# Optimization experiments

Hardware: AMD Instinct MI355X
Metric: run time of the kernel (lower is better)

The kernel has to match this reference:

```python
import jax, jax.numpy as jnp
import numpy as np

N_EMBD = 1024
N_HEAD = 16
B, T = 4, 2048


def setup_inputs() -> dict:
    key = jax.random.key(0)
    ks = jax.random.split(key, 9)
    s = 1.0 / np.sqrt(N_EMBD)
    d = dict(
        x=jax.random.normal(ks[0], (B, T, N_EMBD), dtype=jnp.float32),
        Wq=jax.random.normal(ks[1], (N_EMBD, N_EMBD), dtype=jnp.float32) * s,
        bq=jax.random.normal(ks[2], (N_EMBD,), dtype=jnp.float32) * 0.01,
        Wk=jax.random.normal(ks[3], (N_EMBD, N_EMBD), dtype=jnp.float32) * s,
        bk=jax.random.normal(ks[4], (N_EMBD,), dtype=jnp.float32) * 0.01,
        Wv=jax.random.normal(ks[5], (N_EMBD, N_EMBD), dtype=jnp.float32) * s,
        bv=jax.random.normal(ks[6], (N_EMBD,), dtype=jnp.float32) * 0.01,
        Wp=jax.random.normal(ks[7], (N_EMBD, N_EMBD), dtype=jnp.float32) * s,
        bp=jax.random.normal(ks[8], (N_EMBD,), dtype=jnp.float32) * 0.01,
    )
    return d


def reference(x, Wq, bq, Wk, bk, Wv, bv, Wp, bp):
    b, t, c = x.shape
    h = N_HEAD
    hd = c // h
    # QKV projections -> [B, H, T, hd]
    def heads(w, bias):
        return (x @ w.T + bias).reshape(b, t, h, hd).transpose(0, 2, 1, 3)
    q = heads(Wq, bq)
    k = heads(Wk, bk)
    v = heads(Wv, bv)
    scale = 1.0 / np.sqrt(hd)
    att = jnp.einsum('bhqd,bhkd->bhqk', q, k) * scale  # [B,H,T,T]
    att = jax.nn.softmax(att, axis=-1)
    y = jnp.einsum('bhqk,bhkd->bhqd', att, v)          # [B,H,T,hd]
    y = y.transpose(0, 2, 1, 3).reshape(b, t, c)
    att_mean = att.mean(axis=1)                        # [B,T,T]
    y = y @ Wp.T + bp
    return y, att_mean
```

## Files before the change

kernel.cpp:

```cpp
#include <hip/hip_runtime.h>
#include <hip/hip_bf16.h>
#include <stdint.h>

#define T_SEQ 2048
#define C_EMB 1024
#define NH    16
#define HD    64
#define BB    4

typedef __attribute__((ext_vector_type(8))) short short8;
typedef __attribute__((ext_vector_type(4))) short short4v;
typedef __attribute__((ext_vector_type(4))) float f32x4;

__device__ __forceinline__ f32x4 mfma16(short8 a, short8 b, f32x4 c) {
  return __builtin_amdgcn_mfma_f32_16x16x32_bf16(a, b, c, 0, 0, 0);
}

__device__ __forceinline__ void load_lds16(const void* g, void* l) {
  __builtin_amdgcn_global_load_lds(
      (__attribute__((address_space(1))) void*)(g),
      (__attribute__((address_space(3))) void*)(l), 16, 0, 0);
}

__device__ __forceinline__ unsigned short f2bf(float f) {
  union { float f; unsigned u; } x; x.f = f;
  unsigned r = x.u + 0x7fffu + ((x.u >> 16) & 1u);
  return (unsigned short)(r >> 16);
}

__device__ __forceinline__ short8 swz_read(const unsigned short* base, int r, int cb) {
  return *(const short8*)((const char*)base + r * 128 + (cb ^ ((r & 7) << 4)));
}

__global__ void cvt4(const float* __restrict__ src, unsigned short* __restrict__ dst, int n) {
  int i = (blockIdx.x * 256 + threadIdx.x) * 4;
  if (i < n) {
    float4 v = *reinterpret_cast<const float4*>(src + i);
    short4v o;
    o[0] = (short)f2bf(v.x); o[1] = (short)f2bf(v.y);
    o[2] = (short)f2bf(v.z); o[3] = (short)f2bf(v.w);
    *reinterpret_cast<short4v*>(dst + i) = o;
  }
}

__global__ void pack_bias(const float* __restrict__ bq, const float* __restrict__ bk,
                          const float* __restrict__ bv, float* __restrict__ out) {
  int i = blockIdx.x * 256 + threadIdx.x;
  float v = (i < 1024) ? bq[i] : (i < 2048 ? bk[i - 1024] : bv[i - 2048]);
  out[i] = v;
}

template <bool OUT_BF16>
__global__ void gemm_bt(const unsigned short* __restrict__ A,
                        const unsigned short* __restrict__ Bw,
                        const float* __restrict__ bias,
                        unsigned short* __restrict__ Cb, float* __restrict__ Cf,
                        int M, int N, int K) {
  __shared__ unsigned short lA[128 * 64];
  __shared__ unsigned short lB[128 * 64];
  const int tid = threadIdx.x;
  const int lane = tid & 63;
  const int w = tid >> 6;
  const int m0 = blockIdx.x * 128;
  const int n0 = blockIdx.y * 128;
  const int wm = (w >> 1) * 64, wn = (w & 1) * 64;

  f32x4 acc[4][4] = {};

  for (int k0 = 0; k0 < K; k0 += 64) {
#pragma unroll
    for (int i = 0; i < 4; ++i) {
      int o = (i * 256 + tid) * 16;
      int row = o >> 7, colb = o & 127;
      load_lds16(A + (size_t)(m0 + row) * K + k0 + (colb >> 1), (char*)lA + o);
      load_lds16(Bw + (size_t)(n0 + row) * K + k0 + (colb >> 1), (char*)lB + o);
    }
    __syncthreads();
#pragma unroll
    for (int kk = 0; kk < 2; ++kk) {
      short8 af[4], bf[4];
#pragma unroll
      for (int mi = 0; mi < 4; ++mi)
        af[mi] = *(const short8*)&lA[(wm + mi * 16 + (lane & 15)) * 64 + kk * 32 + (lane >> 4) * 8];
#pragma unroll
      for (int ni = 0; ni < 4; ++ni)
        bf[ni] = *(const short8*)&lB[(wn + ni * 16 + (lane & 15)) * 64 + kk * 32 + (lane >> 4) * 8];
#pragma unroll
      for (int mi = 0; mi < 4; ++mi)
#pragma unroll
        for (int ni = 0; ni < 4; ++ni)
          acc[mi][ni] = mfma16(af[mi], bf[ni], acc[mi][ni]);
    }
    __syncthreads();
  }
#pragma unroll
  for (int mi = 0; mi < 4; ++mi) {
#pragma unroll
    for (int ni = 0; ni < 4; ++ni) {
#pragma unroll
      for (int r = 0; r < 4; ++r) {
        int m = m0 + wm + mi * 16 + (lane >> 4) * 4 + r;
        int n = n0 + wn + ni * 16 + (lane & 15);
        float v = acc[mi][ni][r] + bias[n];
        if (OUT_BF16) Cb[(size_t)m * N + n] = f2bf(v);
        else          Cf[(size_t)m * N + n] = v;
      }
    }
  }
}

__global__ void vtrans(const unsigned short* __restrict__ qkv, unsigned short* __restrict__ vt) {
  const int tt = blockIdx.x, h = blockIdx.y, b = blockIdx.z;
  const int tid = threadIdx.x;
  __shared__ unsigned short ltile[64][65];
#pragma unroll
  for (int i = 0; i < 2; ++i) {
    int e = i * 2048 + tid * 8;
    int t = e >> 6, d = e & 63;
    short8 v = *(const short8*)(qkv + ((size_t)(b * T_SEQ + tt * 64 + t)) * 3072 + 2048 + h * 64 + d);
#pragma unroll
    for (int j = 0; j < 8; ++j) ltile[d + j][t] = (unsigned short)v[j];
  }
  __syncthreads();
#pragma unroll
  for (int i = 0; i < 2; ++i) {
    int e = i * 2048 + tid * 8;
    int d = e >> 6, t = e & 63;
    short8 sv;
#pragma unroll
    for (int j = 0; j < 8; ++j) sv[j] = (short)ltile[d][t + j];
    *(short8*)(vt + ((size_t)((b * NH + h) * HD + d)) * T_SEQ + tt * 64 + t) = sv;
  }
}

__global__ void flash_fwd(const unsigned short* __restrict__ qkv,
                          const unsigned short* __restrict__ vt,
                          unsigned short* __restrict__ yb,
                          float* __restrict__ mstat, float* __restrict__ lstat) {
  const int qt = blockIdx.x, h = blockIdx.y, b = blockIdx.z;
  const int tid = threadIdx.x, lane = tid & 63, w = tid >> 6;
  __shared__ unsigned short kl[2][64 * 64];
  __shared__ unsigned short vl[2][64 * 64];
  __shared__ unsigned short pl[4][16 * 64];
  const int qbase = qt * 64;
  const float scale = 0.125f;

  short8 qf[2];
  {
    int qr = qbase + w * 16 + (lane & 15);
    const unsigned short* qp = qkv + ((size_t)(b * T_SEQ + qr)) * 3072 + h * 64 + (lane >> 4) * 8;
    qf[0] = *(const short8*)(qp);
    qf[1] = *(const short8*)(qp + 32);
  }

  f32x4 yacc[4] = {};
  float mrow[4], lrow[4];
#pragma unroll
  for (int r = 0; r < 4; ++r) { mrow[r] = -1e30f; lrow[r] = 0.f; }

  auto stage = [&](int buf, int kb) {
#pragma unroll
    for (int i = 0; i < 2; ++i) {
      int o = (i * 256 + tid) * 16;
      int row = o >> 7;
      int colb = (o & 127) ^ ((row & 7) << 4);
      load_lds16(qkv + ((size_t)(b * T_SEQ + kb + row)) * 3072 + 1024 + h * 64 + (colb >> 1),
                 (char*)kl[buf] + o);
      load_lds16(vt + ((size_t)((b * NH + h) * HD + row)) * T_SEQ + kb + (colb >> 1),
                 (char*)vl[buf] + o);
    }
  };

  stage(0, 0);
  __syncthreads();
  int cur = 0;

  for (int kt = 0; kt < T_SEQ / 64; ++kt) {
    if (kt + 1 < T_SEQ / 64) stage(cur ^ 1, (kt + 1) * 64);

    f32x4 s[4] = {};
#pragma unroll
    for (int kk = 0; kk < 2; ++kk) {
#pragma unroll
      for (int ct = 0; ct < 4; ++ct) {
        short8 bfr = swz_read(kl[cur], ct * 16 + (lane & 15), kk * 64 + (lane >> 4) * 16);
        s[ct] = mfma16(qf[kk], bfr, s[ct]);
      }
    }

    float alpha[4];
#pragma unroll
    for (int r = 0; r < 4; ++r) {
      float mx = fmaxf(fmaxf(s[0][r], s[1][r]), fmaxf(s[2][r], s[3][r]));
#pragma unroll
      for (int d = 1; d < 16; d <<= 1) mx = fmaxf(mx, __shfl_xor(mx, d));
      float mt = mx * scale;
      float mnew = fmaxf(mrow[r], mt);
      alpha[r] = __expf(mrow[r] - mnew);
      mrow[r] = mnew;
      float sum = 0.f;
      int pr = (lane >> 4) * 4 + r;
#pragma unroll
      for (int ct = 0; ct < 4; ++ct) {
        float p = __expf(s[ct][r] * scale - mnew);
        sum += p;
        *(unsigned short*)((char*)pl[w] + pr * 128 +
                           ((ct * 32 + (lane & 15) * 2) ^ ((pr & 7) << 4))) = f2bf(p);
      }
#pragma unroll
      for (int d = 1; d < 16; d <<= 1) sum += __shfl_xor(sum, d);
      lrow[r] = lrow[r] * alpha[r] + sum;
    }
#pragma unroll
    for (int dt = 0; dt < 4; ++dt)
#pragma unroll
      for (int r = 0; r < 4; ++r) yacc[dt][r] *= alpha[r];

#pragma unroll
    for (int kk = 0; kk < 2; ++kk) {
      short8 pa = swz_read(pl[w], lane & 15, kk * 64 + (lane >> 4) * 16);
#pragma unroll
      for (int dt = 0; dt < 4; ++dt) {
        short8 bv = swz_read(vl[cur], dt * 16 + (lane & 15), kk * 64 + (lane >> 4) * 16);
        yacc[dt] = mfma16(pa, bv, yacc[dt]);
      }
    }

    __syncthreads();
    cur ^= 1;
  }

#pragma unroll
  for (int r = 0; r < 4; ++r) {
    int qr = qbase + w * 16 + (lane >> 4) * 4 + r;
    float inv = 1.f / lrow[r];
#pragma unroll
    for (int dt = 0; dt < 4; ++dt) {
      float v = yacc[dt][r] * inv;
      yb[((size_t)(b * T_SEQ + qr)) * C_EMB + h * HD + dt * 16 + (lane & 15)] = f2bf(v);
    }
    if ((lane & 15) == 0) {
      mstat[(size_t)(b * NH + h) * T_SEQ + qr] = mrow[r];
      lstat[(size_t)(b * NH + h) * T_SEQ + qr] = inv;
    }
  }
}

__global__ void att_mean_k(const unsigned short* __restrict__ qkv,
                           const float* __restrict__ mstat, const float* __restrict__ lstat,
                           float* __restrict__ am) {
  const int ktb = blockIdx.x, qt = blockIdx.y, b = blockIdx.z;
  const int tid = threadIdx.x, lane = tid & 63, w = tid >> 6;
  __shared__ unsigned short kl[2][64 * 64];
  __shared__ float sm[16][64], sl[16][64];
  const float scale = 0.125f;

  auto stage = [&](int buf, int h) {
#pragma unroll
    for (int i = 0; i < 2; ++i) {
      int o = (i * 256 + tid) * 16;
      int row = o >> 7;
      int colb = (o & 127) ^ ((row & 7) << 4);
      load_lds16(qkv + ((size_t)(b * T_SEQ + ktb * 64 + row)) * 3072 + 1024 + h * 64 + (colb >> 1),
                 (char*)kl[buf] + o);
    }
  };

  for (int i = tid; i < 16 * 64; i += 256) {
    int h = i >> 6, q = i & 63;
    sm[h][q] = mstat[(size_t)(b * NH + h) * T_SEQ + qt * 64 + q];
    sl[h][q] = lstat[(size_t)(b * NH + h) * T_SEQ + qt * 64 + q];
  }

  stage(0, 0);
  __syncthreads();
  int cur = 0;

  f32x4 acc[4] = {};
  for (int h = 0; h < NH; ++h) {
    if (h + 1 < NH) stage(cur ^ 1, h + 1);

    short8 qf0, qf1;
    {
      int qr = qt * 64 + w * 16 + (lane & 15);
      const unsigned short* qp = qkv + ((size_t)(b * T_SEQ + qr)) * 3072 + h * 64 + (lane >> 4) * 8;
      qf0 = *(const short8*)qp;
      qf1 = *(const short8*)(qp + 32);
    }

    f32x4 s[4] = {};
#pragma unroll
    for (int ct = 0; ct < 4; ++ct) {
      short8 b0 = swz_read(kl[cur], ct * 16 + (lane & 15), (lane >> 4) * 16);
      s[ct] = mfma16(qf0, b0, s[ct]);
      short8 b1 = swz_read(kl[cur], ct * 16 + (lane & 15), 64 + (lane >> 4) * 16);
      s[ct] = mfma16(qf1, b1, s[ct]);
    }
#pragma unroll
    for (int r = 0; r < 4; ++r) {
      int q = w * 16 + (lane >> 4) * 4 + r;
      float mh = sm[h][q], ilh = sl[h][q];
#pragma unroll
      for (int ct = 0; ct < 4; ++ct)
        acc[ct][r] += __expf(s[ct][r] * scale - mh) * ilh;
    }
    __syncthreads();
    cur ^= 1;
  }

#pragma unroll
  for (int r = 0; r < 4; ++r) {
    int q = qt * 64 + w * 16 + (lane >> 4) * 4 + r;
#pragma unroll
    for (int ct = 0; ct < 4; ++ct)
      am[((size_t)(b * T_SEQ) + q) * T_SEQ + ktb * 64 + ct * 16 + (lane & 15)] = acc[ct][r] * (1.f / 16.f);
  }
}

extern "C" void kernel_launch(void* const* d_in, const int* in_sizes, int n_in,
                              void* d_out, int out_size, void* d_ws, size_t ws_size,
                              hipStream_t stream) {
  const float* x  = (const float*)d_in[0];
  const float* Wq = (const float*)d_in[1];
  const float* bq = (const float*)d_in[2];
  const float* Wk = (const float*)d_in[3];
  const float* bk = (const float*)d_in[4];
  const float* Wv = (const float*)d_in[5];
  const float* bv = (const float*)d_in[6];
  const float* Wp = (const float*)d_in[7];
  const float* bp = (const float*)d_in[8];

  char* ws = (char*)d_ws;
  size_t off = 0;
  auto alloc = [&](size_t bytes) { void* p = ws + off; off += (bytes + 255) & ~(size_t)255; return p; };
  unsigned short* xb   = (unsigned short*)alloc((size_t)8192 * 1024 * 2);
  unsigned short* wqkv = (unsigned short*)alloc((size_t)3 * 1024 * 1024 * 2);
  unsigned short* wpb  = (unsigned short*)alloc((size_t)1024 * 1024 * 2);
  unsigned short* qkvb = (unsigned short*)alloc((size_t)8192 * 3072 * 2);
  unsigned short* vtb  = (unsigned short*)alloc((size_t)BB * NH * HD * T_SEQ * 2);
  unsigned short* ybf  = (unsigned short*)alloc((size_t)8192 * 1024 * 2);
  float* bqkv = (float*)alloc(3072 * 4);
  float* mst  = (float*)alloc((size_t)BB * NH * T_SEQ * 4);
  float* lst  = (float*)alloc((size_t)BB * NH * T_SEQ * 4);

  float* y_out  = (float*)d_out;
  float* am_out = y_out + (size_t)8192 * 1024;

  cvt4<<<8192, 256, 0, stream>>>(x, xb, 8388608);
  cvt4<<<1024, 256, 0, stream>>>(Wq, wqkv, 1048576);
  cvt4<<<1024, 256, 0, stream>>>(Wk, wqkv + 1048576, 1048576);
  cvt4<<<1024, 256, 0, stream>>>(Wv, wqkv + 2097152, 1048576);
  cvt4<<<1024, 256, 0, stream>>>(Wp, wpb, 1048576);
  pack_bias<<<12, 256, 0, stream>>>(bq, bk, bv, bqkv);

  gemm_bt<true><<<dim3(64, 24), 256, 0, stream>>>(xb, wqkv, bqkv, qkvb, nullptr, 8192, 3072, 1024);
  vtrans<<<dim3(32, 16, 4), 256, 0, stream>>>(qkvb, vtb);
  flash_fwd<<<dim3(32, 16, 4), 256, 0, stream>>>(qkvb, vtb, ybf, mst, lst);
  att_mean_k<<<dim3(32, 32, 4), 256, 0, stream>>>(qkvb, mst, lst, am_out);
  gemm_bt<false><<<dim3(64, 8), 256, 0, stream>>>(ybf, wpb, bp, nullptr, y_out, 8192, 1024, 1024);
}
```

Before: 551.7 us.

## Rewrite flash attention with 32x32 MFMA, register P, and lazy rescaling

The flash attention kernel now gives each wave 32 query rows and uses 32x32x16 bf16 MFMAs computing S transposed (K·Q), so P stays in registers and is repacked by lane shuffles instead of going through LDS. Softmax moves to the exp2 domain with a folded scale constant. The running max is updated only when a tile's max exceeds it by a threshold, which skips most of the accumulator rescaling. Query tiles per block double, halving the grid, and MFMA regions are wrapped in setprio hints; the lazy rescale bounds intermediate growth to about 2^11.5, and att_mean is switched to the same log2-domain statistics.

```diff
diff --git a/kernel.cpp b/kernel.cpp
--- a/kernel.cpp
+++ b/kernel.cpp
@@ -11,9 +11,13 @@
 typedef __attribute__((ext_vector_type(8))) short short8;
 typedef __attribute__((ext_vector_type(4))) short short4v;
 typedef __attribute__((ext_vector_type(4))) float f32x4;
+typedef __attribute__((ext_vector_type(16))) float f32x16;
 
 __device__ __forceinline__ f32x4 mfma16(short8 a, short8 b, f32x4 c) {
   return __builtin_amdgcn_mfma_f32_16x16x32_bf16(a, b, c, 0, 0, 0);
+}
+__device__ __forceinline__ f32x16 mfma32(short8 a, short8 b, f32x16 c) {
+  return __builtin_amdgcn_mfma_f32_32x32x16_bf16(a, b, c, 0, 0, 0);
 }
 
 __device__ __forceinline__ void load_lds16(const void* g, void* l) {
@@ -27,10 +31,19 @@
   unsigned r = x.u + 0x7fffu + ((x.u >> 16) & 1u);
   return (unsigned short)(r >> 16);
 }
+__device__ __forceinline__ unsigned pack_bf16(float lo, float hi) {
+  return (unsigned)f2bf(lo) | ((unsigned)f2bf(hi) << 16);
+}
+
+__device__ __forceinline__ float half_max(float x) { return fmaxf(x, __shfl_xor(x, 32)); }
+__device__ __forceinline__ float half_add(float x) { return x + __shfl_xor(x, 32); }
 
 __device__ __forceinline__ short8 swz_read(const unsigned short* base, int r, int cb) {
   return *(const short8*)((const char*)base + r * 128 + (cb ^ ((r & 7) << 4)));
 }
+
+#define C2LOG 0.1803368801111f
+#define THR2  11.5f
 
 __global__ void cvt4(const float* __restrict__ src, unsigned short* __restrict__ dst, int n) {
   int i = (blockIdx.x * 256 + threadIdx.x) * 4;
@@ -139,24 +152,21 @@
                           float* __restrict__ mstat, float* __restrict__ lstat) {
   const int qt = blockIdx.x, h = blockIdx.y, b = blockIdx.z;
   const int tid = threadIdx.x, lane = tid & 63, w = tid >> 6;
+  const int hi = lane >> 5, lq = lane & 31;
   __shared__ unsigned short kl[2][64 * 64];
   __shared__ unsigned short vl[2][64 * 64];
-  __shared__ unsigned short pl[4][16 * 64];
-  const int qbase = qt * 64;
-  const float scale = 0.125f;
-
-  short8 qf[2];
+  const int qwave = qt * 128 + w * 32;
+
+  short8 qf[4];
   {
-    int qr = qbase + w * 16 + (lane & 15);
-    const unsigned short* qp = qkv + ((size_t)(b * T_SEQ + qr)) * 3072 + h * 64 + (lane >> 4) * 8;
-    qf[0] = *(const short8*)(qp);
-    qf[1] = *(const short8*)(qp + 32);
-  }
-
-  f32x4 yacc[4] = {};
-  float mrow[4], lrow[4];
-#pragma unroll
-  for (int r = 0; r < 4; ++r) { mrow[r] = -1e30f; lrow[r] = 0.f; }
+    const unsigned short* qp = qkv + ((size_t)(b * T_SEQ + qwave + lq)) * 3072 + h * 64 + hi * 8;
+#pragma unroll
+    for (int dstep = 0; dstep < 4; ++dstep)
+      qf[dstep] = *(const short8*)(qp + dstep * 16);
+  }
+
+  f32x16 yacc[2] = {};
+  float m2 = -3.0e38f, l = 0.f;
 
   auto stage = [&](int buf, int kb) {
 #pragma unroll
@@ -178,71 +188,92 @@
   for (int kt = 0; kt < T_SEQ / 64; ++kt) {
     if (kt + 1 < T_SEQ / 64) stage(cur ^ 1, (kt + 1) * 64);
 
-    f32x4 s[4] = {};
-#pragma unroll
-    for (int kk = 0; kk < 2; ++kk) {
-#pragma unroll
-      for (int ct = 0; ct < 4; ++ct) {
-        short8 bfr = swz_read(kl[cur], ct * 16 + (lane & 15), kk * 64 + (lane >> 4) * 16);
-        s[ct] = mfma16(qf[kk], bfr, s[ct]);
-      }
-    }
-
-    float alpha[4];
-#pragma unroll
-    for (int r = 0; r < 4; ++r) {
-      float mx = fmaxf(fmaxf(s[0][r], s[1][r]), fmaxf(s[2][r], s[3][r]));
-#pragma unroll
-      for (int d = 1; d < 16; d <<= 1) mx = fmaxf(mx, __shfl_xor(mx, d));
-      float mt = mx * scale;
-      float mnew = fmaxf(mrow[r], mt);
-      alpha[r] = __expf(mrow[r] - mnew);
-      mrow[r] = mnew;
-      float sum = 0.f;
-      int pr = (lane >> 4) * 4 + r;
-#pragma unroll
-      for (int ct = 0; ct < 4; ++ct) {
-        float p = __expf(s[ct][r] * scale - mnew);
-        sum += p;
-        *(unsigned short*)((char*)pl[w] + pr * 128 +
-                           ((ct * 32 + (lane & 15) * 2) ^ ((pr & 7) << 4))) = f2bf(p);
-      }
-#pragma unroll
-      for (int d = 1; d < 16; d <<= 1) sum += __shfl_xor(sum, d);
-      lrow[r] = lrow[r] * alpha[r] + sum;
-    }
-#pragma unroll
-    for (int dt = 0; dt < 4; ++dt)
-#pragma unroll
-      for (int r = 0; r < 4; ++r) yacc[dt][r] *= alpha[r];
-
-#pragma unroll
-    for (int kk = 0; kk < 2; ++kk) {
-      short8 pa = swz_read(pl[w], lane & 15, kk * 64 + (lane >> 4) * 16);
-#pragma unroll
-      for (int dt = 0; dt < 4; ++dt) {
-        short8 bv = swz_read(vl[cur], dt * 16 + (lane & 15), kk * 64 + (lane >> 4) * 16);
-        yacc[dt] = mfma16(pa, bv, yacc[dt]);
-      }
+#pragma unroll
+    for (int ksc = 0; ksc < 2; ++ksc) {
+      f32x16 s = {};
+      __builtin_amdgcn_s_setprio(1);
+#pragma unroll
+      for (int dstep = 0; dstep < 4; ++dstep) {
+        short8 kf = swz_read(kl[cur], ksc * 32 + lq, dstep * 32 + hi * 16);
+        s = mfma32(kf, qf[dstep], s);
+      }
+      __builtin_amdgcn_s_setprio(0);
+
+      float px = fmaxf(fmaxf(fmaxf(s[0], s[1]), fmaxf(s[2], s[3])),
+                       fmaxf(fmaxf(s[4], s[5]), fmaxf(s[6], s[7])));
+      float px2 = fmaxf(fmaxf(fmaxf(s[8], s[9]), fmaxf(s[10], s[11])),
+                        fmaxf(fmaxf(s[12], s[13]), fmaxf(s[14], s[15])));
+      px = half_max(fmaxf(px, px2)) * C2LOG;
+
+      if (!__all(px <= m2 + THR2)) {
+        float mnew = fmaxf(m2, px);
+        float alpha = exp2f(m2 - mnew);
+#pragma unroll
+        for (int r = 0; r < 16; ++r) {
+          float ar = __shfl(alpha, (r & 3) + 8 * (r >> 2) + 4 * hi);
+          yacc[0][r] *= ar;
+          yacc[1][r] *= ar;
+        }
+        l *= alpha;
+        m2 = mnew;
+      }
+
+      float p[16];
+#pragma unroll
+      for (int r = 0; r < 16; ++r) p[r] = exp2f(fmaf(s[r], C2LOG, -m2));
+      float rs = (((p[0] + p[1]) + (p[2] + p[3])) + ((p[4] + p[5]) + (p[6] + p[7]))) +
+                 (((p[8] + p[9]) + (p[10] + p[11])) + ((p[12] + p[13]) + (p[14] + p[15])));
+      l += half_add(rs);
+
+      unsigned w0[4], w1[4];
+#pragma unroll
+      for (int c = 0; c < 4; ++c) {
+        w0[c] = pack_bf16(p[4 * c], p[4 * c + 1]);
+        w1[c] = pack_bf16(p[4 * c + 2], p[4 * c + 3]);
+      }
+      short8 pa[2];
+#pragma unroll
+      for (int ks = 0; ks < 2; ++ks) {
+        unsigned x0 = w0[2 * ks], x1 = w0[2 * ks + 1];
+        unsigned y0 = w1[2 * ks], y1 = w1[2 * ks + 1];
+        unsigned px0 = __shfl_xor(x0, 32), px1 = __shfl_xor(x1, 32);
+        unsigned py0 = __shfl_xor(y0, 32), py1 = __shfl_xor(y1, 32);
+        union { unsigned u[4]; short8 s8; } fu;
+        fu.u[0] = hi ? px1 : x0;
+        fu.u[1] = hi ? py1 : y0;
+        fu.u[2] = hi ? x1  : px0;
+        fu.u[3] = hi ? y1  : py0;
+        pa[ks] = fu.s8;
+      }
+
+      __builtin_amdgcn_s_setprio(1);
+#pragma unroll
+      for (int dtile = 0; dtile < 2; ++dtile) {
+#pragma unroll
+        for (int ks = 0; ks < 2; ++ks) {
+          short8 vf = swz_read(vl[cur], dtile * 32 + lq, ksc * 64 + ks * 32 + hi * 16);
+          yacc[dtile] = mfma32(pa[ks], vf, yacc[dtile]);
+        }
+      }
+      __builtin_amdgcn_s_setprio(0);
     }
 
     __syncthreads();
     cur ^= 1;
   }
 
-#pragma unroll
-  for (int r = 0; r < 4; ++r) {
-    int qr = qbase + w * 16 + (lane >> 4) * 4 + r;
-    float inv = 1.f / lrow[r];
-#pragma unroll
-    for (int dt = 0; dt < 4; ++dt) {
-      float v = yacc[dt][r] * inv;
-      yb[((size_t)(b * T_SEQ + qr)) * C_EMB + h * HD + dt * 16 + (lane & 15)] = f2bf(v);
-    }
-    if ((lane & 15) == 0) {
-      mstat[(size_t)(b * NH + h) * T_SEQ + qr] = mrow[r];
-      lstat[(size_t)(b * NH + h) * T_SEQ + qr] = inv;
-    }
+  float inv = 1.f / l;
+#pragma unroll
+  for (int r = 0; r < 16; ++r) {
+    int qrow = (r & 3) + 8 * (r >> 2) + 4 * hi;
+    float ir = __shfl(inv, qrow);
+    size_t base = ((size_t)(b * T_SEQ + qwave + qrow)) * C_EMB + h * 64 + lq;
+    yb[base]      = f2bf(yacc[0][r] * ir);
+    yb[base + 32] = f2bf(yacc[1][r] * ir);
+  }
+  if (lane < 32) {
+    mstat[(size_t)(b * NH + h) * T_SEQ + qwave + lq] = m2;
+    lstat[(size_t)(b * NH + h) * T_SEQ + qwave + lq] = inv;
   }
 }
 
@@ -253,7 +284,6 @@
   const int tid = threadIdx.x, lane = tid & 63, w = tid >> 6;
   __shared__ unsigned short kl[2][64 * 64];
   __shared__ float sm[16][64], sl[16][64];
-  const float scale = 0.125f;
 
   auto stage = [&](int buf, int h) {
 #pragma unroll
@@ -302,7 +332,7 @@
       float mh = sm[h][q], ilh = sl[h][q];
 #pragma unroll
       for (int ct = 0; ct < 4; ++ct)
-        acc[ct][r] += __expf(s[ct][r] * scale - mh) * ilh;
+        acc[ct][r] += exp2f(fmaf(s[ct][r], C2LOG, -mh)) * ilh;
     }
     __syncthreads();
     cur ^= 1;
@@ -355,7 +385,7 @@
 
   gemm_bt<true><<<dim3(64, 24), 256, 0, stream>>>(xb, wqkv, bqkv, qkvb, nullptr, 8192, 3072, 1024);
   vtrans<<<dim3(32, 16, 4), 256, 0, stream>>>(qkvb, vtb);
-  flash_fwd<<<dim3(32, 16, 4), 256, 0, stream>>>(qkvb, vtb, ybf, mst, lst);
+  flash_fwd<<<dim3(16, 16, 4), 256, 0, stream>>>(qkvb, vtb, ybf, mst, lst);
   att_mean_k<<<dim3(32, 32, 4), 256, 0, stream>>>(qkvb, mst, lst, am_out);
   gemm_bt<false><<<dim3(64, 8), 256, 0, stream>>>(ybf, wpb, bp, nullptr, y_out, 8192, 1024, 1024);
 }
```

After: 473.0 us. 14.3% less time.
